# Kernel tuning notes

Hardware: AMD Instinct MI355X
Metric: run time of the kernel (lower is better)

Reference implementation:

```python
import jax, jax.numpy as jnp
import numpy as np
import math

S = 72; IMG_W = 640; IMG_H = 360; STRIDE = 16
IN_CH = 256; AFC = 64
FMAP_H = IMG_H // STRIDE  # 22
FMAP_W = IMG_W // STRIDE  # 40
N_OFFSETS = S
LEFT_ANGLES = [72., 60., 49., 39., 30., 22.]
RIGHT_ANGLES = [108., 120., 131., 141., 150., 158.]
BOTTOM_ANGLES = [165., 150., 141., 131., 120., 108., 100., 90., 80., 72., 60., 49., 39., 30., 15.]
BATCH = 8


def _gen_anchor(start, angle, cut):
    n = FMAP_H if cut else N_OFFSETS
    ys = np.linspace(1., 0., n)
    a = np.zeros(5 + n)
    sx, sy = start
    a[2] = 1. - sy
    a[3] = sx
    a[5:] = (sx + (1. - ys - 1. + sy) / math.tan(angle * math.pi / 180.)) * IMG_W
    return a


def _gen_side(angles, nb, x=None, y=None):
    if x is None:
        starts = [(xx, y) for xx in np.linspace(1., 0., nb)]
    else:
        starts = [(x, yy) for yy in np.linspace(1., 0., nb)]
    anc = np.stack([_gen_anchor(s, a, False) for s in starts for a in angles])
    cut = np.stack([_gen_anchor(s, a, True) for s in starts for a in angles])
    return anc, cut


def build_anchor_tables():
    la, lc = _gen_side(LEFT_ANGLES, 72, x=0.)
    ra, rc = _gen_side(RIGHT_ANGLES, 72, x=1.)
    ba, bc = _gen_side(BOTTOM_ANGLES, 128, y=1.)
    anchors = np.concatenate([la, ba, ra]).astype(np.float32)  # [P, 5+S]
    cuts = np.concatenate([lc, bc, rc])                        # [P, 5+fmap_h]
    xs = np.flip(np.round(cuts[:, 5:] / STRIDE), axis=1).astype(np.int64)
    cut_xs = np.clip(xs, 0, FMAP_W - 1).astype(np.int32)       # [P, fmap_h]
    invalid = (xs < 0) | (xs > FMAP_W)                         # faithful to original (> not >=)
    return anchors, cut_xs, invalid


def setup_inputs():
    key = jax.random.key(0)
    ks = jax.random.split(key, 6)
    anchors, cut_xs, invalid = build_anchor_tables()
    P = anchors.shape[0]  # 2784
    D = AFC * FMAP_H      # 1408
    s = 0.02
    return {
        "x": jax.random.normal(ks[0], (BATCH, IN_CH, FMAP_H, FMAP_W), jnp.float32),
        "conv_w": jax.random.normal(ks[1], (AFC, IN_CH), jnp.float32) * s,
        "conv_b": jnp.zeros((AFC,), jnp.float32),
        "att_w": jax.random.normal(ks[2], (P - 1, D), jnp.float32) * s,
        "att_b": jnp.zeros((P - 1,), jnp.float32),
        "cls_w": jax.random.normal(ks[3], (2, 2 * D), jnp.float32) * s,
        "cls_b": jnp.zeros((2,), jnp.float32),
        "so_w": jax.random.normal(ks[4], (1, 2 * D), jnp.float32) * s,
        "so_b": jnp.zeros((1,), jnp.float32),
        "reg_w": jax.random.normal(ks[5], (N_OFFSETS + 1, 2 * D), jnp.float32) * s,
        "reg_b": jnp.zeros((N_OFFSETS + 1,), jnp.float32),
        "anchors": jnp.asarray(anchors),
        "cut_xs": jnp.asarray(cut_xs),
        "invalid_mask": jnp.asarray(invalid),
    }


def reference(x, conv_w, conv_b, att_w, att_b, cls_w, cls_b, so_w, so_b, reg_w, reg_b, anchors, cut_xs, invalid_mask):
    B = x.shape[0]
    P, H = cut_xs.shape
    # 1x1 conv
    feat = jnp.einsum('bchw,oc->bohw', x, conv_w) + conv_b[None, :, None, None]
    # fused anchor feature gather: rois[b,p,c,h] = feat[b,c,h,cut_xs[p,h]]
    rois = feat[:, :, jnp.arange(H)[None, :], cut_xs]           # [B,C,P,H]
    rois = jnp.transpose(rois, (0, 2, 1, 3))                    # [B,P,C,H]
    rois = jnp.where(invalid_mask[None, :, None, :], 0., rois)
    D = rois.shape[2] * H
    baf = rois.reshape(B, P, D)
    scores = baf.reshape(B * P, D) @ att_w.T + att_b
    attention = jax.nn.softmax(scores, axis=1).reshape(B, P, P - 1)
    # off-diagonal scatter (replaces torch eye/nonzero trick): M[b,i,j]=attention[b,i,j'] for j!=i, diag 0
    i_idx = jnp.arange(P)[:, None]
    j_off = jnp.arange(P - 1)[None, :]
    tgt_j = jnp.where(j_off < i_idx, j_off, j_off + 1)          # [P,P-1]
    M = jnp.zeros((B, P, P), x.dtype).at[:, jnp.broadcast_to(i_idx, (P, P - 1)), tgt_j].set(attention)
    # (baf^T @ M^T)^T == M @ baf
    att_feats = jnp.einsum('bpq,bqd->bpd', M, baf)
    feats = jnp.concatenate([att_feats, baf], axis=2).reshape(B * P, 2 * D)
    cls = (feats @ cls_w.T + cls_b).reshape(B, P, 2)
    so = jax.nn.sigmoid(feats @ so_w.T + so_b).reshape(B, P, 1)
    reg = (feats @ reg_w.T + reg_b).reshape(B, P, N_OFFSETS + 1)
    anc = jnp.broadcast_to(anchors[None], (B, P, anchors.shape[1]))
    reg_proposals = jnp.concatenate([cls, (anc[:, :, 2:3] + so) * 0.5, anc[:, :, 3:4], anc[:, :, 4:] + reg], axis=2)
    return reg_proposals, M, feat
```

## Files before the change

kernel.cpp:

```cpp
#include <hip/hip_runtime.h>
#include <stdint.h>

#define PTOT 2784
#define PM1  2783
#define DDIM 1408
#define NB   8
#define ROWS 22272
#define KHEAD 2816
#define MROW 2816
#define BTROWS 1536

typedef __attribute__((ext_vector_type(8))) short bf16x8;
typedef __attribute__((ext_vector_type(4))) float f32x4;
typedef long i64f8;

__device__ __forceinline__ short f2bf_rne(float x) {
    uint32_t u = __float_as_uint(x);
    u += 0x7fffu + ((u >> 16) & 1u);
    return (short)(u >> 16);
}
__device__ __forceinline__ float bf2f(short s) {
    return __uint_as_float((uint32_t)(unsigned short)s << 16);
}

__device__ __forceinline__ unsigned char f2e4m3(float x) {
    uint32_t u = __float_as_uint(x);
    uint32_t sgn = (u >> 24) & 0x80u;
    uint32_t ax = u & 0x7fffffffu;
    ax += 0x7ffffu + ((ax >> 20) & 1u);
    if (ax >= 0x43E80000u) return (unsigned char)(sgn | 0x7Eu);
    if (ax < 0x3C800000u) return (unsigned char)sgn;
    uint32_t e = (ax >> 23) - 120u;
    uint32_t m = (ax >> 20) & 7u;
    return (unsigned char)(sgn | (e << 3) | m);
}

__device__ __forceinline__ void gld16(const void* g, void* l) {
    __builtin_amdgcn_global_load_lds(
        (const __attribute__((address_space(1))) void*)(uintptr_t)g,
        (__attribute__((address_space(3))) void*)(uint32_t)(uintptr_t)l,
        16, 0, 0);
}

#define VMW(N) asm volatile("s_waitcnt vmcnt(" #N ")" ::: "memory")

__global__ __launch_bounds__(256) void k_conv(
    const float* __restrict__ x, const float* __restrict__ w,
    const float* __restrict__ cb, float* __restrict__ feat) {
  __shared__ float xs[256 * 32];
  int b = blockIdx.x / 28;
  int t0 = (blockIdx.x % 28) * 32;
  int t = threadIdx.x;
  for (int i = t; i < 256 * 32; i += 256) {
    int c = i >> 5, pos = i & 31;
    int hw = t0 + pos;
    xs[i] = (hw < 880) ? x[((size_t)b * 256 + c) * 880 + hw] : 0.f;
  }
  __syncthreads();
  int o = t & 63, g = t >> 6;
  float acc[8];
#pragma unroll
  for (int pp = 0; pp < 8; ++pp) acc[pp] = cb[o];
  const float* wr = w + o * 256;
  for (int c = 0; c < 256; ++c) {
    float wv = wr[c];
#pragma unroll
    for (int pp = 0; pp < 8; ++pp) acc[pp] += wv * xs[c * 32 + g + pp * 4];
  }
#pragma unroll
  for (int pp = 0; pp < 8; ++pp) {
    int hw = t0 + g + pp * 4;
    if (hw < 880) feat[((size_t)b * 64 + o) * 880 + hw] = acc[pp];
  }
}

__global__ __launch_bounds__(256) void k_prep(
    const float* __restrict__ att_w, const float* __restrict__ cls_w,
    const float* __restrict__ so_w, const float* __restrict__ reg_w,
    const float* __restrict__ cls_b, const float* __restrict__ so_b,
    const float* __restrict__ reg_b,
    short* __restrict__ attw, short* __restrict__ wbf,
    float* __restrict__ bias80, float* __restrict__ M,
    unsigned char* __restrict__ Mbf8, unsigned char* __restrict__ bafT8,
    short* __restrict__ Msc) {
  const int64_t n_attw = (int64_t)2816 * DDIM;
  const int64_t n_w = 80 * (int64_t)KHEAD;
  const int64_t n_pa = (int64_t)NB * MROW * 32;
  const int64_t n_pb = (int64_t)NB * BTROWS * 32;
  const int64_t total = n_attw + n_w + 80 + ROWS + n_pa + n_pb;
  for (int64_t i = (int64_t)blockIdx.x * 256 + threadIdx.x; i < total;
       i += (int64_t)gridDim.x * 256) {
    if (i < n_attw) {
      int j = (int)(i / DDIM), k = (int)(i - (int64_t)j * DDIM);
      float v = (j < PM1) ? att_w[(size_t)j * DDIM + k] : 0.f;
      attw[i] = f2bf_rne(v);
    } else if (i < n_attw + n_w) {
      int64_t ii = i - n_attw;
      int n = (int)(ii / KHEAD), k = (int)(ii - (int64_t)n * KHEAD);
      float v = 0.f;
      if (n < 2) v = cls_w[n * KHEAD + k];
      else if (n == 2) v = so_w[k];
      else if (n < 76) v = reg_w[(size_t)(n - 3) * KHEAD + k];
      wbf[ii] = f2bf_rne(v);
    } else if (i < n_attw + n_w + 80) {
      int n = (int)(i - n_attw - n_w);
      float v = 0.f;
      if (n < 2) v = cls_b[n];
      else if (n == 2) v = so_b[0];
      else if (n < 76) v = reg_b[n - 3];
      bias80[n] = v;
    } else if (i < n_attw + n_w + 80 + ROWS) {
      int r = (int)(i - n_attw - n_w - 80);
      int p = r % PTOT;
      M[(size_t)r * PTOT + p] = -1e30f;
      if (Msc) Msc[(size_t)r * PTOT + p] = f2bf_rne(-1e30f);
    } else if (i < n_attw + n_w + 80 + ROWS + n_pa) {
      int64_t ii = i - n_attw - n_w - 80 - ROWS;
      int64_t row = ii >> 5; int c = (int)(ii & 31);
      Mbf8[row * 2816 + 2784 + c] = 0;
    } else {
      int64_t ii = i - n_attw - n_w - 80 - ROWS - n_pa;
      int64_t row = ii >> 5; int c = (int)(ii & 31);
      bafT8[row * 2816 + 2784 + c] = 0;
    }
  }
}

__global__ __launch_bounds__(256) void k_gather(
    const float* __restrict__ feat, const int* __restrict__ cutx,
    const unsigned char* __restrict__ inval,
    short* __restrict__ baf, unsigned char* __restrict__ bafT8) {
  int p0 = blockIdx.x * 64, d0 = blockIdx.y * 64, b = blockIdx.z;
  __shared__ short tile[64][72];
  int t = threadIdx.x;
  for (int i = t; i < 64 * 64; i += 256) {
    int pl = i >> 6, dl = i & 63;
    int p = p0 + pl, d = d0 + dl;
    float v = 0.f;
    if (p < PTOT && d < DDIM) {
      int c = d / 22, h = d - c * 22;
      if (!inval[p * 22 + h]) {
        int xc = cutx[p * 22 + h];
        v = feat[(((size_t)b * 64 + c) * 22 + h) * 40 + xc];
      }
    }
    tile[pl][dl] = f2bf_rne(v);
  }
  __syncthreads();
  if (d0 < DDIM) {
    for (int u = t; u < 512; u += 256) {
      int pl = u >> 3, dg = u & 7;
      int p = p0 + pl;
      if (p < PTOT) {
        bf16x8 v;
#pragma unroll
        for (int e = 0; e < 8; ++e) v[e] = tile[pl][dg * 8 + e];
        *(bf16x8*)&baf[((size_t)b * PTOT + p) * DDIM + d0 + dg * 8] = v;
      }
    }
  }
  for (int u = t; u < 512; u += 256) {
    int dl = u >> 3, pg = u & 7;
    int pbase = p0 + pg * 8;
    if (pbase + 7 < PTOT) {
      unsigned long long pk = 0;
#pragma unroll
      for (int e = 0; e < 8; ++e) {
        float fv = bf2f(tile[pg * 8 + e][dl]);
        pk |= (unsigned long long)f2e4m3(fv) << (8 * e);
      }
      *(unsigned long long*)&bafT8[((size_t)b * BTROWS + d0 + dl) * 2816 + pbase] = pk;
    }
  }
}

#define SC_TILE(OFF_, S_, SN_, STAGE_, VM_)                                    \
  {                                                                            \
    const char* cb_ = sm + (S_) * 24576;                                       \
    if (STAGE_) {                                                              \
      char* nb_ = sm + (SN_) * 24576;                                          \
      gld16(gA0 + (OFF_), nb_ + ddA);                                          \
      gld16(gB0 + (OFF_), nb_ + 8192 + ddA);                                   \
      gld16(gB1 + (OFF_), nb_ + 16384 + ddA);                                  \
    }                                                                          \
    if ((VM_) == 6) VMW(6); else if ((VM_) == 3) VMW(3); else VMW(0);          \
    __builtin_amdgcn_s_barrier();                                              \
    bf16x8 av[4], bv[4];                                                       \
    _Pragma("unroll") for (int i = 0; i < 4; ++i)                              \
      av[i] = *(const bf16x8*)(cb_ + offA[i]);                                 \
    _Pragma("unroll") for (int i = 0; i < 4; ++i)                              \
      bv[i] = *(const bf16x8*)(cb_ + 8192 + offB[i]);                          \
    _Pragma("unroll") for (int mi = 0; mi < 4; ++mi)                           \
      _Pragma("unroll") for (int ni = 0; ni < 4; ++ni)                         \
        acc[mi][ni] = __builtin_amdgcn_mfma_f32_16x16x32_bf16(                 \
            av[mi], bv[ni], acc[mi][ni], 0, 0, 0);                             \
    __builtin_amdgcn_s_barrier();                                              \
  }

template<int OUTMODE>
__global__ __launch_bounds__(512, 4) void k_scores(
    const short* __restrict__ baf, const short* __restrict__ attw,
    const float* __restrict__ att_b, float* __restrict__ Mout,
    short* __restrict__ Msc) {
  __shared__ char sm[73728];
  int wg = blockIdx.x;
  int xcd = wg & 7, lin = wg >> 3;
  int wgid = (xcd < 2) ? xcd * 240 + lin : 480 + (xcd - 2) * 239 + lin;
  int it = wgid / 11, nt = wgid - it * 11;
  int m0 = it * 128, n0 = nt * 256;

  int t = threadIdx.x, w = t >> 6, l = t & 63;
  int lr = l & 15, lg = l >> 4;
  int wr = w >> 2, wc = w & 3;

  const char* gA0; const char* gB0; const char* gB1;
  int ddA = t * 16;
  {
    int oA = t * 16;
    int rA = oA >> 6, cA = (oA & 63) ^ (((oA >> 7) & 3) << 4);
    gA0 = (const char*)(baf + (size_t)(m0 + rA) * DDIM) + cA;
    int oB0 = t * 16;
    int rB0 = oB0 >> 6, cB0 = (oB0 & 63) ^ (((oB0 >> 7) & 3) << 4);
    gB0 = (const char*)(attw + (size_t)(n0 + rB0) * DDIM) + cB0;
    int oB1 = 8192 + t * 16;
    int rB1 = oB1 >> 6, cB1 = (oB1 & 63) ^ (((oB1 >> 7) & 3) << 4);
    gB1 = (const char*)(attw + (size_t)(n0 + rB1) * DDIM) + cB1;
  }
  int offA[4], offB[4];
#pragma unroll
  for (int i = 0; i < 4; ++i) {
    int xa = (wr * 64 + i * 16 + lr) * 64 + lg * 16;
    offA[i] = xa ^ (((xa >> 7) & 3) << 4);
    int xb = (wc * 64 + i * 16 + lr) * 64 + lg * 16;
    offB[i] = xb ^ (((xb >> 7) & 3) << 4);
  }

  f32x4 acc[4][4];
  const f32x4 fz = {0.f, 0.f, 0.f, 0.f};
#pragma unroll
  for (int mi = 0; mi < 4; ++mi)
#pragma unroll
    for (int ni = 0; ni < 4; ++ni) acc[mi][ni] = fz;

  gld16(gA0, sm + ddA);
  gld16(gB0, sm + 8192 + ddA);
  gld16(gB1, sm + 16384 + ddA);
  gld16(gA0 + 64, sm + 24576 + ddA);
  gld16(gB0 + 64, sm + 24576 + 8192 + ddA);
  gld16(gB1 + 64, sm + 24576 + 16384 + ddA);

  for (int q = 0; q < 14; ++q) {
    SC_TILE(128, 0, 2, 1, 6);
    SC_TILE(192, 1, 0, 1, 6);
    SC_TILE(256, 2, 1, 1, 6);
    gA0 += 192; gB0 += 192; gB1 += 192;
  }
  SC_TILE(0, 0, 0, 0, 3);
  SC_TILE(0, 1, 0, 0, 0);

#pragma unroll
  for (int mi = 0; mi < 4; ++mi) {
#pragma unroll
    for (int rg = 0; rg < 4; ++rg) {
      int gmi = m0 + wr * 64 + mi * 16 + lg * 4 + rg;
      int i = gmi % PTOT;
#pragma unroll
      for (int ni = 0; ni < 4; ++ni) {
        int j = n0 + wc * 64 + ni * 16 + lr;
        if (j < PM1) {
          int q2 = j + (j >= i);
          float v = acc[mi][ni][rg] + att_b[j];
          if (OUTMODE == 0) Mout[(size_t)gmi * PTOT + q2] = v;
          else              Msc[(size_t)gmi * PTOT + q2] = f2bf_rne(v);
        }
      }
    }
  }
}

#define AF_TILE(OFF_, S_, SN_, STAGE_, VM_)                                    \
  {                                                                            \
    const char* cb_ = sm + (S_) * 24576;                                       \
    if (STAGE_) {                                                              \
      char* nb_ = sm + (SN_) * 24576;                                          \
      gld16(gA0 + (OFF_), nb_ + ddA);                                          \
      gld16(gB0 + (OFF_), nb_ + 8192 + ddA);                                   \
      gld16(gB1 + (OFF_), nb_ + 16384 + ddA);                                  \
    }                                                                          \
    if ((VM_) == 6) VMW(6); else if ((VM_) == 3) VMW(3); else VMW(0);          \
    __builtin_amdgcn_s_barrier();                                              \
    _Pragma("unroll") for (int ks = 0; ks < 2; ++ks) {                         \
      i64f8 av[4], bv[4];                                                      \
      _Pragma("unroll") for (int i = 0; i < 4; ++i)                            \
        av[i] = *(const i64f8*)(cb_ + offA[i * 2 + ks]);                       \
      _Pragma("unroll") for (int i = 0; i < 4; ++i)                            \
        bv[i] = *(const i64f8*)(cb_ + 8192 + offB[i * 2 + ks]);                \
      _Pragma("unroll") for (int mi = 0; mi < 4; ++mi)                         \
        _Pragma("unroll") for (int ni = 0; ni < 4; ++ni)                       \
          acc[mi][ni] = __builtin_amdgcn_mfma_f32_16x16x32_fp8_fp8(            \
              av[mi], bv[ni], acc[mi][ni], 0, 0, 0);                           \
    }                                                                          \
    __builtin_amdgcn_s_barrier();                                              \
  }

__global__ __launch_bounds__(512, 4) void k_attfeat8(
    const unsigned char* __restrict__ Mbf8,
    const unsigned char* __restrict__ bafT8,
    short* __restrict__ attf) {
  __shared__ char sm[73728];
  int wg = blockIdx.x;
  int wgid = (wg & 7) * 132 + (wg >> 3);
  int bb = wgid / 132;
  int rem = wgid - bb * 132;
  int it = rem / 6, dt = rem - it * 6;
  int m0 = it * 128, n0 = dt * 256;
  const unsigned char* Ab = Mbf8 + ((size_t)bb * MROW + m0) * 2816;
  const unsigned char* Bb = bafT8 + ((size_t)bb * BTROWS + n0) * 2816;

  int t = threadIdx.x, w = t >> 6, l = t & 63;
  int lr = l & 15, lg = l >> 4;
  int wr = w >> 2, wc = w & 3;

  const char* gA0; const char* gB0; const char* gB1;
  int ddA = t * 16;
  {
    int oA = t * 16;
    int rA = oA >> 6, cA = (oA & 63) ^ (((oA >> 7) & 3) << 4);
    gA0 = (const char*)Ab + (size_t)rA * 2816 + cA;
    int oB0 = t * 16;
    int rB0 = oB0 >> 6, cB0 = (oB0 & 63) ^ (((oB0 >> 7) & 3) << 4);
    gB0 = (const char*)Bb + (size_t)rB0 * 2816 + cB0;
    int oB1 = 8192 + t * 16;
    int rB1 = oB1 >> 6, cB1 = (oB1 & 63) ^ (((oB1 >> 7) & 3) << 4);
    gB1 = (const char*)Bb + (size_t)rB1 * 2816 + cB1;
  }
  int offA[8], offB[8];
#pragma unroll
  for (int i = 0; i < 4; ++i) {
#pragma unroll
    for (int ks = 0; ks < 2; ++ks) {
      int xa = (wr * 64 + i * 16 + lr) * 64 + ks * 32 + lg * 8;
      offA[i * 2 + ks] = xa ^ (((xa >> 7) & 3) << 4);
      int xb = (wc * 64 + i * 16 + lr) * 64 + ks * 32 + lg * 8;
      offB[i * 2 + ks] = xb ^ (((xb >> 7) & 3) << 4);
    }
  }

  f32x4 acc[4][4];
  const f32x4 fz = {0.f, 0.f, 0.f, 0.f};
#pragma unroll
  for (int mi = 0; mi < 4; ++mi)
#pragma unroll
    for (int ni = 0; ni < 4; ++ni) acc[mi][ni] = fz;

  gld16(gA0, sm + ddA);
  gld16(gB0, sm + 8192 + ddA);
  gld16(gB1, sm + 16384 + ddA);
  gld16(gA0 + 64, sm + 24576 + ddA);
  gld16(gB0 + 64, sm + 24576 + 8192 + ddA);
  gld16(gB1 + 64, sm + 24576 + 16384 + ddA);

  for (int q = 0; q < 14; ++q) {
    AF_TILE(128, 0, 2, 1, 6);
    AF_TILE(192, 1, 0, 1, 6);
    AF_TILE(256, 2, 1, 1, 6);
    gA0 += 192; gB0 += 192; gB1 += 192;
  }
  AF_TILE(0, 0, 0, 0, 3);
  AF_TILE(0, 1, 0, 0, 0);

  const float US = 1.0f / 1024.0f;
#pragma unroll
  for (int mi = 0; mi < 4; ++mi) {
#pragma unroll
    for (int rg = 0; rg < 4; ++rg) {
      int i = m0 + wr * 64 + mi * 16 + lg * 4 + rg;
      if (i < PTOT) {
        short* arow = attf + ((size_t)(bb * PTOT + i)) * DDIM;
#pragma unroll
        for (int ni = 0; ni < 4; ++ni) {
          int d = n0 + wc * 64 + ni * 16 + lr;
          if (d < DDIM) arow[d] = f2bf_rne(acc[mi][ni][rg] * US);
        }
      }
    }
  }
}

template<int INMODE>
__global__ __launch_bounds__(256) void k_softmax(float* __restrict__ M,
                                                 unsigned char* __restrict__ Mbf8,
                                                 const short* __restrict__ Msc) {
  __shared__ float red[8];
  int r = blockIdx.x;
  int b = r / PTOT, p = r - b * PTOT;
  float* pr = M + (size_t)r * PTOT;
  const short* ms = INMODE ? (Msc + (size_t)r * PTOT) : (const short*)nullptr;
  unsigned char* mb = Mbf8 + ((size_t)b * MROW + p) * 2816;
  int t = threadIdx.x;
  bool has2 = (t < 348 - 256);
  float v0[8], v1[8];
  float mx = -3.0e38f;
  if (INMODE == 0) {
    f32x4 a0 = *(const f32x4*)(pr + t * 8);
    f32x4 a1 = *(const f32x4*)(pr + t * 8 + 4);
#pragma unroll
    for (int e = 0; e < 4; ++e) { v0[e] = a0[e]; v0[4 + e] = a1[e]; }
  } else {
    bf16x8 a = *(const bf16x8*)(ms + t * 8);
#pragma unroll
    for (int e = 0; e < 8; ++e) v0[e] = bf2f(a[e]);
  }
#pragma unroll
  for (int e = 0; e < 8; ++e) mx = fmaxf(mx, v0[e]);
  if (has2) {
    if (INMODE == 0) {
      f32x4 b0 = *(const f32x4*)(pr + (256 + t) * 8);
      f32x4 b1 = *(const f32x4*)(pr + (256 + t) * 8 + 4);
#pragma unroll
      for (int e = 0; e < 4; ++e) { v1[e] = b0[e]; v1[4 + e] = b1[e]; }
    } else {
      bf16x8 bb = *(const bf16x8*)(ms + (256 + t) * 8);
#pragma unroll
      for (int e = 0; e < 8; ++e) v1[e] = bf2f(bb[e]);
    }
#pragma unroll
    for (int e = 0; e < 8; ++e) mx = fmaxf(mx, v1[e]);
  }
#pragma unroll
  for (int off = 32; off; off >>= 1) mx = fmaxf(mx, __shfl_xor(mx, off));
  if ((t & 63) == 0) red[t >> 6] = mx;
  __syncthreads();
  mx = fmaxf(fmaxf(red[0], red[1]), fmaxf(red[2], red[3]));
  float s = 0.f;
#pragma unroll
  for (int e = 0; e < 8; ++e) { v0[e] = __expf(v0[e] - mx); s += v0[e]; }
  if (has2) {
#pragma unroll
    for (int e = 0; e < 8; ++e) { v1[e] = __expf(v1[e] - mx); s += v1[e]; }
  }
#pragma unroll
  for (int off = 32; off; off >>= 1) s += __shfl_xor(s, off);
  if ((t & 63) == 0) red[4 + (t >> 6)] = s;
  __syncthreads();
  s = (red[4] + red[5]) + (red[6] + red[7]);
  float inv = 1.f / s;
  float invs = inv * 1024.f;
  {
    f32x4 o0, o1; unsigned long long pk = 0;
#pragma unroll
    for (int e = 0; e < 8; ++e) {
      float wv = v0[e] * inv;
      if (e < 4) o0[e] = wv; else o1[e - 4] = wv;
      pk |= (unsigned long long)f2e4m3(v0[e] * invs) << (8 * e);
    }
    *(f32x4*)(pr + t * 8) = o0;
    *(f32x4*)(pr + t * 8 + 4) = o1;
    *(unsigned long long*)(mb + t * 8) = pk;
  }
  if (has2) {
    f32x4 o0, o1; unsigned long long pk = 0;
#pragma unroll
    for (int e = 0; e < 8; ++e) {
      float wv = v1[e] * inv;
      if (e < 4) o0[e] = wv; else o1[e - 4] = wv;
      pk |= (unsigned long long)f2e4m3(v1[e] * invs) << (8 * e);
    }
    *(f32x4*)(pr + (256 + t) * 8) = o0;
    *(f32x4*)(pr + (256 + t) * 8 + 4) = o1;
    *(unsigned long long*)(mb + (256 + t) * 8) = pk;
  }
}

__global__ __launch_bounds__(256) void k_head(
    const short* __restrict__ attf, const short* __restrict__ baf,
    const short* __restrict__ wbf, const float* __restrict__ bias80,
    const float* __restrict__ anch, float* __restrict__ out) {
  __shared__ short smA[64 * 32];
  __shared__ short smB[80 * 32];
  int r0 = blockIdx.x * 64;
  int t = threadIdx.x, wid = t >> 6, lane = t & 63;
  int rowa = t >> 2, kg = t & 3;
  const short* sA_att = attf + (size_t)(r0 + rowa) * DDIM + kg * 8;
  const short* sA_baf = baf + (size_t)(r0 + rowa) * DDIM + kg * 8;
  const short* sB0 = wbf + (size_t)rowa * KHEAD + kg * 8;
  const short* sB1 = wbf + (size_t)(64 + (t >> 2)) * KHEAD + (t & 3) * 8;
  char* lA = (char*)smA + wid * 1024;
  char* lB0 = (char*)smB + wid * 1024;
  char* lB1 = (char*)smB + 4096;
  int lr = lane & 15, lg = lane >> 4;
  const short* pA = smA + (wid * 16 + lr) * 32 + lg * 8;
  const short* pB = smB + lr * 32 + lg * 8;
  f32x4 acc[5];
  const f32x4 fz = {0.f, 0.f, 0.f, 0.f};
  for (int i2 = 0; i2 < 5; ++i2) acc[i2] = fz;
  for (int ks = 0; ks < 88; ++ks) {
    const short* sA = (ks < 44) ? (sA_att + ks * 32) : (sA_baf + (ks - 44) * 32);
    gld16(sA, lA);
    gld16(sB0 + ks * 32, lB0);
    if (t < 64) gld16(sB1 + ks * 32, lB1);
    __syncthreads();
    bf16x8 a = *(const bf16x8*)pA;
#pragma unroll
    for (int ni = 0; ni < 5; ++ni) {
      bf16x8 b = *(const bf16x8*)(pB + ni * 512);
      acc[ni] = __builtin_amdgcn_mfma_f32_16x16x32_bf16(a, b, acc[ni], 0, 0, 0);
    }
    __syncthreads();
  }
#pragma unroll
  for (int ni = 0; ni < 5; ++ni) {
#pragma unroll
    for (int rg = 0; rg < 4; ++rg) {
      int n = ni * 16 + lr;
      int i = wid * 16 + lg * 4 + rg;
      int rgl = r0 + i;
      int p = rgl % PTOT;
      float v = acc[ni][rg] + bias80[n];
      if (n < 2) {
        out[(size_t)rgl * 77 + n] = v;
      } else if (n == 2) {
        out[(size_t)rgl * 77 + 2] =
            (anch[(size_t)p * 77 + 2] + 1.f / (1.f + __expf(-v))) * 0.5f;
        out[(size_t)rgl * 77 + 3] = anch[(size_t)p * 77 + 3];
      } else if (n < 76) {
        out[(size_t)rgl * 77 + n + 1] = v + anch[(size_t)p * 77 + n + 1];
      }
    }
  }
}

extern "C" void kernel_launch(void* const* d_in, const int* in_sizes, int n_in,
                              void* d_out, int out_size, void* d_ws, size_t ws_size,
                              hipStream_t stream) {
  const float* x      = (const float*)d_in[0];
  const float* conv_w = (const float*)d_in[1];
  const float* conv_b = (const float*)d_in[2];
  const float* att_w  = (const float*)d_in[3];
  const float* att_b  = (const float*)d_in[4];
  const float* cls_w  = (const float*)d_in[5];
  const float* cls_b  = (const float*)d_in[6];
  const float* so_w   = (const float*)d_in[7];
  const float* so_b   = (const float*)d_in[8];
  const float* reg_w  = (const float*)d_in[9];
  const float* reg_b  = (const float*)d_in[10];
  const float* anchors= (const float*)d_in[11];
  const int*   cut_xs = (const int*)d_in[12];
  const unsigned char* invalid = (const unsigned char*)d_in[13];

  float* out_rp = (float*)d_out;
  float* Mmat = out_rp + (size_t)ROWS * 77;
  float* feat = Mmat + (size_t)ROWS * PTOT;

  char* wsp = (char*)d_ws;
  short* baf            = (short*)wsp;
  unsigned char* bafT8  = (unsigned char*)(wsp + 62717952ULL);
  unsigned char* Mbf8   = (unsigned char*)(wsp + 97320960ULL);
  short* attw           = (short*)(wsp + 160759808ULL);
  short* wbf            = (short*)(wsp + 168689664ULL);
  float* bias80         = (float*)(wsp + 169140224ULL);
  short* attf           = (short*)(wsp + 169140736ULL);
  short* Msc            = (short*)(wsp + 231858688ULL);
  const size_t WS_FAST  = 231858688ULL + 124010496ULL;

  bool fast = (ws_size >= WS_FAST);

  k_conv<<<224, 256, 0, stream>>>(x, conv_w, conv_b, feat);
  k_prep<<<2048, 256, 0, stream>>>(att_w, cls_w, so_w, reg_w, cls_b, so_b, reg_b,
                                   attw, wbf, bias80, Mmat, Mbf8, bafT8,
                                   fast ? Msc : (short*)nullptr);
  k_gather<<<dim3(44, 24, 8), 256, 0, stream>>>(feat, cut_xs, invalid, baf, bafT8);
  if (fast) {
    k_scores<1><<<1914, 512, 0, stream>>>(baf, attw, att_b, (float*)nullptr, Msc);
    k_softmax<1><<<ROWS, 256, 0, stream>>>(Mmat, Mbf8, Msc);
  } else {
    k_scores<0><<<1914, 512, 0, stream>>>(baf, attw, att_b, Mmat, (short*)nullptr);
    k_softmax<0><<<ROWS, 256, 0, stream>>>(Mmat, Mbf8, (const short*)nullptr);
  }
  k_attfeat8<<<1056, 512, 0, stream>>>(Mbf8, bafT8, attf);
  k_head<<<348, 256, 0, stream>>>(attf, baf, wbf, bias80, anchors, out_rp);
}
```

Before: 637.2 us.

## Permute fp8 K layout for 16-byte LDS reads and pipeline head GEMM loads

Reorders the fp8 K dimension of the attention-weight matrix and transposed features in 64-byte groups, so each lane reads both MFMA k-steps with one 16-byte LDS load instead of two 8-byte loads. All writers (pad zeroing, gather, softmax output) apply the same permutation, which keeps the dot product unchanged. Separately, the head kernel gets a three-stage async global-to-LDS pipeline with counted vmcnt waits in place of the load-then-syncthreads loop. The aim is fewer LDS instructions and less load-latency stall, at the cost of more LDS use in the head kernel and fragile per-wave wait counts.

```diff
diff --git a/kernel.cpp b/kernel.cpp
--- a/kernel.cpp
+++ b/kernel.cpp
@@ -13,6 +13,7 @@
 typedef __attribute__((ext_vector_type(8))) short bf16x8;
 typedef __attribute__((ext_vector_type(4))) float f32x4;
 typedef long i64f8;
+typedef __attribute__((ext_vector_type(2))) long i64x2;
 
 __device__ __forceinline__ short f2bf_rne(float x) {
     uint32_t u = __float_as_uint(x);
@@ -33,6 +34,10 @@
     uint32_t e = (ax >> 23) - 120u;
     uint32_t m = (ax >> 20) & 7u;
     return (unsigned char)(sgn | (e << 3) | m);
+}
+
+__device__ __forceinline__ size_t kperm(size_t c) {
+    return (c & ~(size_t)63) + (((c >> 3) & 3) << 4) + (((c >> 5) & 1) << 3) + (c & 7);
 }
 
 __device__ __forceinline__ void gld16(const void* g, void* l) {
@@ -117,11 +122,11 @@
     } else if (i < n_attw + n_w + 80 + ROWS + n_pa) {
       int64_t ii = i - n_attw - n_w - 80 - ROWS;
       int64_t row = ii >> 5; int c = (int)(ii & 31);
-      Mbf8[row * 2816 + 2784 + c] = 0;
+      Mbf8[row * 2816 + kperm(2784 + c)] = 0;
     } else {
       int64_t ii = i - n_attw - n_w - 80 - ROWS - n_pa;
       int64_t row = ii >> 5; int c = (int)(ii & 31);
-      bafT8[row * 2816 + 2784 + c] = 0;
+      bafT8[row * 2816 + kperm(2784 + c)] = 0;
     }
   }
 }
@@ -169,7 +174,8 @@
         float fv = bf2f(tile[pg * 8 + e][dl]);
         pk |= (unsigned long long)f2e4m3(fv) << (8 * e);
       }
-      *(unsigned long long*)&bafT8[((size_t)b * BTROWS + d0 + dl) * 2816 + pbase] = pk;
+      *(unsigned long long*)&bafT8[((size_t)b * BTROWS + d0 + dl) * 2816 +
+                                   kperm(pbase)] = pk;
     }
   }
 }
@@ -289,17 +295,16 @@
     }                                                                          \
     if ((VM_) == 6) VMW(6); else if ((VM_) == 3) VMW(3); else VMW(0);          \
     __builtin_amdgcn_s_barrier();                                              \
-    _Pragma("unroll") for (int ks = 0; ks < 2; ++ks) {                         \
-      i64f8 av[4], bv[4];                                                      \
-      _Pragma("unroll") for (int i = 0; i < 4; ++i)                            \
-        av[i] = *(const i64f8*)(cb_ + offA[i * 2 + ks]);                       \
-      _Pragma("unroll") for (int i = 0; i < 4; ++i)                            \
-        bv[i] = *(const i64f8*)(cb_ + 8192 + offB[i * 2 + ks]);                \
+    i64x2 aw[4], bw[4];                                                        \
+    _Pragma("unroll") for (int i = 0; i < 4; ++i)                              \
+      aw[i] = *(const i64x2*)(cb_ + offA[i]);                                  \
+    _Pragma("unroll") for (int i = 0; i < 4; ++i)                              \
+      bw[i] = *(const i64x2*)(cb_ + 8192 + offB[i]);                           \
+    _Pragma("unroll") for (int ks = 0; ks < 2; ++ks)                           \
       _Pragma("unroll") for (int mi = 0; mi < 4; ++mi)                         \
         _Pragma("unroll") for (int ni = 0; ni < 4; ++ni)                       \
           acc[mi][ni] = __builtin_amdgcn_mfma_f32_16x16x32_fp8_fp8(            \
-              av[mi], bv[ni], acc[mi][ni], 0, 0, 0);                           \
-    }                                                                          \
+              aw[mi][ks], bw[ni][ks], acc[mi][ni], 0, 0, 0);                   \
     __builtin_amdgcn_s_barrier();                                              \
   }
 
@@ -334,16 +339,13 @@
     int rB1 = oB1 >> 6, cB1 = (oB1 & 63) ^ (((oB1 >> 7) & 3) << 4);
     gB1 = (const char*)Bb + (size_t)rB1 * 2816 + cB1;
   }
-  int offA[8], offB[8];
+  int offA[4], offB[4];
 #pragma unroll
   for (int i = 0; i < 4; ++i) {
-#pragma unroll
-    for (int ks = 0; ks < 2; ++ks) {
-      int xa = (wr * 64 + i * 16 + lr) * 64 + ks * 32 + lg * 8;
-      offA[i * 2 + ks] = xa ^ (((xa >> 7) & 3) << 4);
-      int xb = (wc * 64 + i * 16 + lr) * 64 + ks * 32 + lg * 8;
-      offB[i * 2 + ks] = xb ^ (((xb >> 7) & 3) << 4);
-    }
+    int xa = (wr * 64 + i * 16 + lr) * 64 + lg * 16;
+    offA[i] = xa ^ (((xa >> 7) & 3) << 4);
+    int xb = (wc * 64 + i * 16 + lr) * 64 + lg * 16;
+    offB[i] = xb ^ (((xb >> 7) & 3) << 4);
   }
 
   f32x4 acc[4][4];
@@ -456,7 +458,7 @@
     }
     *(f32x4*)(pr + t * 8) = o0;
     *(f32x4*)(pr + t * 8 + 4) = o1;
-    *(unsigned long long*)(mb + t * 8) = pk;
+    *(unsigned long long*)(mb + kperm((size_t)t * 8)) = pk;
   }
   if (has2) {
     f32x4 o0, o1; unsigned long long pk = 0;
@@ -468,7 +470,7 @@
     }
     *(f32x4*)(pr + (256 + t) * 8) = o0;
     *(f32x4*)(pr + (256 + t) * 8 + 4) = o1;
-    *(unsigned long long*)(mb + (256 + t) * 8) = pk;
+    *(unsigned long long*)(mb + kperm((size_t)(256 + t) * 8)) = pk;
   }
 }
 
@@ -476,44 +478,59 @@
     const short* __restrict__ attf, const short* __restrict__ baf,
     const short* __restrict__ wbf, const float* __restrict__ bias80,
     const float* __restrict__ anch, float* __restrict__ out) {
-  __shared__ short smA[64 * 32];
-  __shared__ short smB[80 * 32];
+  __shared__ char sm[27648];
   int r0 = blockIdx.x * 64;
-  int t = threadIdx.x, wid = t >> 6, lane = t & 63;
-  int rowa = t >> 2, kg = t & 3;
-  const short* sA_att = attf + (size_t)(r0 + rowa) * DDIM + kg * 8;
-  const short* sA_baf = baf + (size_t)(r0 + rowa) * DDIM + kg * 8;
-  const short* sB0 = wbf + (size_t)rowa * KHEAD + kg * 8;
-  const short* sB1 = wbf + (size_t)(64 + (t >> 2)) * KHEAD + (t & 3) * 8;
-  char* lA = (char*)smA + wid * 1024;
-  char* lB0 = (char*)smB + wid * 1024;
-  char* lB1 = (char*)smB + 4096;
+  int t = threadIdx.x, w = t >> 6, lane = t & 63;
   int lr = lane & 15, lg = lane >> 4;
-  const short* pA = smA + (wid * 16 + lr) * 32 + lg * 8;
-  const short* pB = smB + lr * 32 + lg * 8;
+  int ddA = t * 16;
+  const char* gA_att = (const char*)(attf + (size_t)(r0 + (t >> 2)) * DDIM) + (t & 3) * 16;
+  const char* gA_baf = (const char*)(baf + (size_t)(r0 + (t >> 2)) * DDIM) + (t & 3) * 16;
+  const char* gB1 = (const char*)(wbf + (size_t)(t >> 2) * KHEAD) + (t & 3) * 16;
+  const char* gB2 = (const char*)(wbf + (size_t)(64 + (t >> 2)) * KHEAD) + (t & 3) * 16;
+  int pAo = (w * 16 + lr) * 64 + lg * 16;
+  int pBo = 4096 + lr * 64 + lg * 16;
   f32x4 acc[5];
   const f32x4 fz = {0.f, 0.f, 0.f, 0.f};
+#pragma unroll
   for (int i2 = 0; i2 < 5; ++i2) acc[i2] = fz;
-  for (int ks = 0; ks < 88; ++ks) {
-    const short* sA = (ks < 44) ? (sA_att + ks * 32) : (sA_baf + (ks - 44) * 32);
-    gld16(sA, lA);
-    gld16(sB0 + ks * 32, lB0);
-    if (t < 64) gld16(sB1 + ks * 32, lB1);
-    __syncthreads();
-    bf16x8 a = *(const bf16x8*)pA;
+
+#pragma unroll
+  for (int s = 0; s < 2; ++s) {
+    char* nb = sm + s * 9216;
+    gld16(gA_att + s * 64, nb + ddA);
+    gld16(gB1 + s * 64, nb + 4096 + ddA);
+    if (t < 64) gld16(gB2 + s * 64, nb + 8192 + ddA);
+  }
+
+#pragma unroll
+  for (int kt = 0; kt < 88; ++kt) {
+    const char* cb_ = sm + (kt % 3) * 9216;
+    int s = kt + 2;
+    if (s < 88) {
+      char* nb_ = sm + (s % 3) * 9216;
+      const char* asrc = (s < 44) ? (gA_att + s * 64) : (gA_baf + (s - 44) * 64);
+      gld16(asrc, nb_ + ddA);
+      gld16(gB1 + s * 64, nb_ + 4096 + ddA);
+      if (t < 64) gld16(gB2 + s * 64, nb_ + 8192 + ddA);
+    }
+    if (w == 0) { if (kt < 86) VMW(6); else if (kt == 86) VMW(3); else VMW(0); }
+    else        { if (kt < 86) VMW(4); else if (kt == 86) VMW(2); else VMW(0); }
+    __builtin_amdgcn_s_barrier();
+    bf16x8 a = *(const bf16x8*)(cb_ + pAo);
 #pragma unroll
     for (int ni = 0; ni < 5; ++ni) {
-      bf16x8 b = *(const bf16x8*)(pB + ni * 512);
-      acc[ni] = __builtin_amdgcn_mfma_f32_16x16x32_bf16(a, b, acc[ni], 0, 0, 0);
-    }
-    __syncthreads();
-  }
+      bf16x8 bvv = *(const bf16x8*)(cb_ + pBo + ni * 1024);
+      acc[ni] = __builtin_amdgcn_mfma_f32_16x16x32_bf16(a, bvv, acc[ni], 0, 0, 0);
+    }
+    __builtin_amdgcn_s_barrier();
+  }
+
 #pragma unroll
   for (int ni = 0; ni < 5; ++ni) {
 #pragma unroll
     for (int rg = 0; rg < 4; ++rg) {
       int n = ni * 16 + lr;
-      int i = wid * 16 + lg * 4 + rg;
+      int i = w * 16 + lg * 4 + rg;
       int rgl = r0 + i;
       int p = rgl % PTOT;
       float v = acc[ni][rg] + bias80[n];
```

Result: faster. 617.6 us (-3.1%).
